# Performance work log

Hardware: AMD Instinct MI355X
Metric: run time of the kernel (lower is better)

The kernel has to match this reference:

```python
import jax, jax.numpy as jnp
import numpy as np

IN_CH = 1024
INTER_CH = 512
NUM_EXPERTS = 128
B, S = 16, 4096  # T = B*S = 65536 tokens, 512 tokens/expert


def setup_inputs() -> dict:
    key = jax.random.key(0)
    kx, kp, k1w, k1b, k2w, k2b, k3w, k3b = jax.random.split(key, 8)
    T = B * S
    x = jax.random.normal(kx, (B, S, IN_CH), dtype=jnp.float32)
    # Mirror torch: indices = randperm(T) % E; idxs = indices.argsort() (stable)
    perm = jax.random.permutation(kp, T)
    expert_assign = perm % NUM_EXPERTS
    idxs = jnp.argsort(expert_assign, stable=True).astype(jnp.int64)
    # BatchLinear params initialized with randn, matching the torch module
    w1_w = jax.random.normal(k1w, (NUM_EXPERTS, INTER_CH, IN_CH), dtype=jnp.float32)
    w1_b = jax.random.normal(k1b, (NUM_EXPERTS, INTER_CH), dtype=jnp.float32)
    w2_w = jax.random.normal(k2w, (NUM_EXPERTS, IN_CH, INTER_CH), dtype=jnp.float32)
    w2_b = jax.random.normal(k2b, (NUM_EXPERTS, IN_CH), dtype=jnp.float32)
    w3_w = jax.random.normal(k3w, (NUM_EXPERTS, INTER_CH, IN_CH), dtype=jnp.float32)
    w3_b = jax.random.normal(k3b, (NUM_EXPERTS, INTER_CH), dtype=jnp.float32)
    return {"x": x, "idxs": idxs, "w1_w": w1_w, "w1_b": w1_b,
            "w2_w": w2_w, "w2_b": w2_b, "w3_w": w3_w, "w3_b": w3_b}


def reference(x, idxs, w1_w, w1_b, w2_w, w2_b, w3_w, w3_b):
    Bx, Sx, C = x.shape
    E = w1_w.shape[0]
    xf = x.reshape(Bx * Sx, C)            # [T, C]
    # dispatch: gather tokens grouped by expert -> [E, T/E, C]
    xs = xf[idxs].reshape(E, -1, C)
    # SwiGLU FFN, batched over experts
    h1 = jnp.einsum('etc,efc->etf', xs, w1_w) + w1_b[:, None, :]  # [E, T/E, F]
    h3 = jnp.einsum('etc,efc->etf', xs, w3_w) + w3_b[:, None, :]
    h = jax.nn.silu(h1) * h3
    out = jnp.einsum('etf,ecf->etc', h, w2_w) + w2_b[:, None, :]  # [E, T/E, C]
    # combine: scatter tokens back to original order
    out = out.reshape(Bx * Sx, C)
    inv = jnp.argsort(idxs)
    return out[inv].reshape(Bx, Sx, C)
```

## Files before the change

### kernel.cpp

```cpp
#include <hip/hip_runtime.h>

#define IN_CH 1024
#define INTER 512
#define NEXP  128
#define TPE   512

typedef __bf16 bf16x8  __attribute__((ext_vector_type(8)));
typedef __bf16 bf16x4v __attribute__((ext_vector_type(4)));
typedef float  f32x4   __attribute__((ext_vector_type(4)));

#define GLOAD(dst, p) \
  asm volatile("global_load_dwordx4 %0, %1, off" : "=&v"(dst) : "v"(p))

#define VM_WAIT() do { \
  asm volatile("s_waitcnt vmcnt(0)" ::: "memory"); \
  __builtin_amdgcn_sched_barrier(0); } while (0)

#define PHASE_SYNC() do { \
  __builtin_amdgcn_s_barrier(); \
  asm volatile("s_waitcnt lgkmcnt(0)" ::: "memory"); \
  __builtin_amdgcn_sched_barrier(0); \
  __builtin_amdgcn_s_setprio(1); } while (0)
#define PHASE_END() do { \
  __builtin_amdgcn_s_setprio(0); \
  __builtin_amdgcn_s_barrier(); } while (0)

#define GLDS16(gsrc, ldst) \
  __builtin_amdgcn_global_load_lds( \
      (const __attribute__((address_space(1))) unsigned int*)(gsrc), \
      (__attribute__((address_space(3))) unsigned int*)(ldst), 16, 0, 0)

__global__ __launch_bounds__(512) void moe_h_kernel(
    const float* __restrict__ x, const int* __restrict__ idxs,
    const float* __restrict__ w1w, const float* __restrict__ w1b,
    const float* __restrict__ w3w, const float* __restrict__ w3b,
    __bf16* __restrict__ hbuf)
{
  __shared__ __align__(16) ushort sA [2][128*64];
  __shared__ __align__(16) ushort sB1[2][128*64];
  __shared__ __align__(16) ushort sB3[2][128*64];

  const int blk = (blockIdx.x & 7) * (NEXP*16/8) + (blockIdx.x >> 3);
  const int e   = blk >> 4;
  const int tl  = blk & 15;
  const int tm  = tl >> 2, tn = tl & 3;

  const int tid  = threadIdx.x;
  const int lane = tid & 63;
  const int wid  = tid >> 6;
  const int wm   = wid >> 1;
  const int wn   = wid & 1;

  const int rA = tid >> 3;
  const int c  = tid & 7;
  const int swzc = ((c ^ (rA&7))<<3);
  const int so0 = rA*64 + swzc;
  const int so1 = (rA+64)*64 + swzc;

  const int tok0 = idxs[e*TPE + tm*128 + rA];
  const int tok1 = idxs[e*TPE + tm*128 + rA + 64];
  const float* ap0 = x + (size_t)tok0*IN_CH + (c<<3);
  const float* ap1 = x + (size_t)tok1*IN_CH + (c<<3);
  const float* q0p = w1w + ((size_t)e*INTER + tn*128 + rA)*IN_CH + (c<<3);
  const float* q1p = q0p + (size_t)64*IN_CH;
  const float* t0p = w3w + ((size_t)e*INTER + tn*128 + rA)*IN_CH + (c<<3);
  const float* t1p = t0p + (size_t)64*IN_CH;

  f32x4 acc1[2][4], acc3[2][4];
#pragma unroll
  for (int a = 0; a < 2; ++a)
#pragma unroll
    for (int b = 0; b < 4; ++b) {
      acc1[a][b] = (f32x4){0.f,0.f,0.f,0.f};
      acc3[a][b] = (f32x4){0.f,0.f,0.f,0.f};
    }

  f32x4 a0l,a0h, a1l,a1h, q0l,q0h, q1l,q1h, t0l,t0h, t1l,t1h;

  auto loads = [&](int kof) {
    GLOAD(a0l, ap0 + kof); GLOAD(a0h, ap0 + kof + 4);
    GLOAD(a1l, ap1 + kof); GLOAD(a1h, ap1 + kof + 4);
    GLOAD(q0l, q0p + kof); GLOAD(q0h, q0p + kof + 4);
    GLOAD(q1l, q1p + kof); GLOAD(q1h, q1p + kof + 4);
    GLOAD(t0l, t0p + kof); GLOAD(t0h, t0p + kof + 4);
    GLOAD(t1l, t1p + kof); GLOAD(t1h, t1p + kof + 4);
  };
  auto cvt8 = [](const f32x4& lo, const f32x4& hi) {
    bf16x8 r;
    r[0]=(__bf16)lo[0]; r[1]=(__bf16)lo[1]; r[2]=(__bf16)lo[2]; r[3]=(__bf16)lo[3];
    r[4]=(__bf16)hi[0]; r[5]=(__bf16)hi[1]; r[6]=(__bf16)hi[2]; r[7]=(__bf16)hi[3];
    return r;
  };
  auto stores = [&](int buf) {
    VM_WAIT();
    *(bf16x8*)&sA [buf][so0] = cvt8(a0l, a0h);
    *(bf16x8*)&sA [buf][so1] = cvt8(a1l, a1h);
    *(bf16x8*)&sB1[buf][so0] = cvt8(q0l, q0h);
    *(bf16x8*)&sB1[buf][so1] = cvt8(q1l, q1h);
    *(bf16x8*)&sB3[buf][so0] = cvt8(t0l, t0h);
    *(bf16x8*)&sB3[buf][so1] = cvt8(t1l, t1h);
  };
  auto mfma_tile = [&](int buf) {
#pragma unroll
    for (int ks = 0; ks < 2; ++ks) {
      bf16x8 af[2], bq[4], bt[4];
      const int k8 = (ks<<2) + (lane>>4);
#pragma unroll
      for (int mi = 0; mi < 2; ++mi) {
        const int r = wm*32 + mi*16 + (lane&15);
        af[mi] = *(const bf16x8*)&sA[buf][r*64 + ((k8 ^ (r&7))<<3)];
      }
#pragma unroll
      for (int ni = 0; ni < 4; ++ni) {
        const int r   = wn*64 + ni*16 + (lane&15);
        const int off = r*64 + ((k8 ^ (r&7))<<3);
        bq[ni] = *(const bf16x8*)&sB1[buf][off];
        bt[ni] = *(const bf16x8*)&sB3[buf][off];
      }
#pragma unroll
      for (int mi = 0; mi < 2; ++mi)
#pragma unroll
        for (int ni = 0; ni < 4; ++ni) {
          acc1[mi][ni] = __builtin_amdgcn_mfma_f32_16x16x32_bf16(af[mi], bq[ni], acc1[mi][ni], 0, 0, 0);
          acc3[mi][ni] = __builtin_amdgcn_mfma_f32_16x16x32_bf16(af[mi], bt[ni], acc3[mi][ni], 0, 0, 0);
        }
    }
  };

  loads(0);
  stores(0);
  loads(64);
  asm volatile("s_waitcnt lgkmcnt(0)" ::: "memory");
  __builtin_amdgcn_s_barrier();

  int cur = 0;
  const int NT = IN_CH/64;
  for (int kt = 0; kt < NT; ++kt) {
    if (kt < NT - 1) stores(cur ^ 1);
    if (kt < NT - 2) loads((kt+2)*64);
    __builtin_amdgcn_s_setprio(1);
    mfma_tile(cur);
    __builtin_amdgcn_s_setprio(0);
    asm volatile("s_waitcnt lgkmcnt(0)" ::: "memory");
    __builtin_amdgcn_s_barrier();
    cur ^= 1;
  }

  const int rowbase = tm*128 + wm*32;
  const int colbase = tn*128 + wn*64;
#pragma unroll
  for (int ni = 0; ni < 4; ++ni) {
    const int fc = colbase + ni*16 + (lane&15);
    const float b1v = w1b[e*INTER + fc];
    const float b3v = w3b[e*INTER + fc];
#pragma unroll
    for (int mi = 0; mi < 2; ++mi) {
#pragma unroll
      for (int j = 0; j < 4; ++j) {
        const int rl = rowbase + mi*16 + ((lane>>4)<<2) + j;
        const float h1 = acc1[mi][ni][j] + b1v;
        const float h3 = acc3[mi][ni][j] + b3v;
        const float s  = h1 / (1.0f + __expf(-h1));
        hbuf[((size_t)e*TPE + rl)*INTER + fc] = (__bf16)(s * h3);
      }
    }
  }
}

__global__ __launch_bounds__(512) void moe_out_kernel(
    const __bf16* __restrict__ hbuf, const float* __restrict__ w2w,
    const float* __restrict__ w2b, const int* __restrict__ idxs,
    float* __restrict__ out)
{
  __shared__ __align__(16) ushort sA[2][128*64];
  __shared__ __align__(16) ushort sB[2][128*64];

  const int blk = (blockIdx.x & 7) * (NEXP*32/8) + (blockIdx.x >> 3);
  const int e   = blk >> 5;
  const int tl  = blk & 31;
  const int tm  = tl >> 3, tn = tl & 7;

  const int tid  = threadIdx.x;
  const int lane = tid & 63;
  const int wid  = tid >> 6;
  const int wm   = wid >> 1;
  const int wn   = wid & 1;

  const int arow0 = wid*16 + (lane>>3);
  const int asc0  = (lane&7) ^ (arow0&7);
  const int asc1  = (lane&7) ^ ((arow0+8)&7);
  const __bf16* ag0 = hbuf + ((size_t)e*TPE + tm*128 + arow0    )*INTER + (asc0<<3);
  const __bf16* ag1 = hbuf + ((size_t)e*TPE + tm*128 + arow0 + 8)*INTER + (asc1<<3);
  const int aslot0 = (wid*128)      * 8;
  const int aslot1 = (wid*128 + 64) * 8;

  const int r0   = tid >> 4;
  const int c4   = tid & 15;
  const int swzB = ((((c4>>1) ^ (r0&7))<<3) | ((c4&1)<<2));
  const float* bp = w2w + ((size_t)e*IN_CH + tn*128 + r0)*INTER + (c4<<2);

  f32x4 acc[2][4];
#pragma unroll
  for (int a = 0; a < 2; ++a)
#pragma unroll
    for (int b = 0; b < 4; ++b) acc[a][b] = (f32x4){0.f,0.f,0.f,0.f};

  float4 wv[4];

  auto gldsA = [&](int buf, int kof) {
    GLDS16(ag0 + kof, &sA[buf][aslot0]);
    GLDS16(ag1 + kof, &sA[buf][aslot1]);
  };
  auto loadsB = [&](int kof) {
#pragma unroll
    for (int i = 0; i < 4; ++i)
      wv[i] = *(const float4*)(bp + (size_t)(32*i)*INTER + kof);
  };
  auto storesB = [&](int buf) {
#pragma unroll
    for (int i = 0; i < 4; ++i) {
      bf16x4v b;
      b[0]=(__bf16)wv[i].x; b[1]=(__bf16)wv[i].y; b[2]=(__bf16)wv[i].z; b[3]=(__bf16)wv[i].w;
      *(bf16x4v*)&sB[buf][(r0 + 32*i)*64 + swzB] = b;
    }
  };
  auto rdA = [&](int buf, int ks, bf16x8 af[2]) {
    const int k8 = (ks<<2) + (lane>>4);
#pragma unroll
    for (int mi = 0; mi < 2; ++mi) {
      const int r = wm*32 + mi*16 + (lane&15);
      af[mi] = *(const bf16x8*)&sA[buf][r*64 + ((k8 ^ (r&7))<<3)];
    }
  };
  auto rdB = [&](int buf, int ks, bf16x8 bfr[4]) {
    const int k8 = (ks<<2) + (lane>>4);
#pragma unroll
    for (int ni = 0; ni < 4; ++ni) {
      const int r = wn*64 + ni*16 + (lane&15);
      bfr[ni] = *(const bf16x8*)&sB[buf][r*64 + ((k8 ^ (r&7))<<3)];
    }
  };

  gldsA(0, 0);
  loadsB(0);
  VM_WAIT();
  storesB(0);
  loadsB(64);
  asm volatile("s_waitcnt lgkmcnt(0)" ::: "memory");
  __builtin_amdgcn_s_barrier();

  int cur = 0;
  const int NT = INTER/64;
  for (int kt = 0; kt < NT; ++kt) {
    bf16x8 af[2], bfr[4];

    rdA(cur, 0, af);
    rdB(cur, 0, bfr);
    if (kt < NT - 1) {
      VM_WAIT();
      storesB(cur ^ 1);
      gldsA(cur ^ 1, (kt+1)*64);
      __builtin_amdgcn_sched_barrier(0);
    }
    if (kt < NT - 2) loadsB((kt+2)*64);
    PHASE_SYNC();
#pragma unroll
    for (int mi = 0; mi < 2; ++mi)
#pragma unroll
      for (int ni = 0; ni < 4; ++ni)
        acc[mi][ni] = __builtin_amdgcn_mfma_f32_16x16x32_bf16(af[mi], bfr[ni], acc[mi][ni], 0, 0, 0);
    PHASE_END();

    rdA(cur, 1, af);
    rdB(cur, 1, bfr);
    PHASE_SYNC();
#pragma unroll
    for (int mi = 0; mi < 2; ++mi)
#pragma unroll
      for (int ni = 0; ni < 4; ++ni)
        acc[mi][ni] = __builtin_amdgcn_mfma_f32_16x16x32_bf16(af[mi], bfr[ni], acc[mi][ni], 0, 0, 0);
    __builtin_amdgcn_s_setprio(0);
    if (kt < NT - 2)      asm volatile("s_waitcnt vmcnt(4)" ::: "memory");
    else if (kt < NT - 1) asm volatile("s_waitcnt vmcnt(0)" ::: "memory");
    __builtin_amdgcn_s_barrier();

    cur ^= 1;
  }

  const int rowbase = tm*128 + wm*32;
  const int colbase = tn*128 + wn*64;
  float b2v[4];
#pragma unroll
  for (int ni = 0; ni < 4; ++ni)
    b2v[ni] = w2b[e*IN_CH + colbase + ni*16 + (lane&15)];
#pragma unroll
  for (int mi = 0; mi < 2; ++mi) {
#pragma unroll
    for (int j = 0; j < 4; ++j) {
      const int rl  = rowbase + mi*16 + ((lane>>4)<<2) + j;
      const int tok = idxs[e*TPE + rl];
      float* orow = out + (size_t)tok*IN_CH;
#pragma unroll
      for (int ni = 0; ni < 4; ++ni)
        orow[colbase + ni*16 + (lane&15)] = acc[mi][ni][j] + b2v[ni];
    }
  }
}

extern "C" void kernel_launch(void* const* d_in, const int* in_sizes, int n_in,
                              void* d_out, int out_size, void* d_ws, size_t ws_size,
                              hipStream_t stream) {
  const float* x    = (const float*)d_in[0];
  const int*   idxs = (const int*)d_in[1];
  const float* w1w  = (const float*)d_in[2];
  const float* w1b  = (const float*)d_in[3];
  const float* w2w  = (const float*)d_in[4];
  const float* w2b  = (const float*)d_in[5];
  const float* w3w  = (const float*)d_in[6];
  const float* w3b  = (const float*)d_in[7];
  float*  out  = (float*)d_out;
  __bf16* hbuf = (__bf16*)d_ws;

  moe_h_kernel<<<dim3(NEXP*16), dim3(512), 0, stream>>>(x, idxs, w1w, w1b, w3w, w3b, hbuf);
  moe_out_kernel<<<dim3(NEXP*32), dim3(512), 0, stream>>>(hbuf, w2w, w2b, idxs, out);
}
```

Before: 483.5 us.

## Pre-convert x to bf16 and use direct-to-LDS gathers with narrower N tiles

Adds a separate pass that converts the whole fp32 activation tensor to bf16 in workspace. The first GEMM kernel can then gather token rows straight into LDS with global_load_lds instead of loading and converting them in registers. The tile shape changes from 128x128 to 128x64 per block, so twice as many blocks run and LDS use is smaller. The cost is an extra full read and write of x (about 384MB of traffic). The new path runs only when the workspace is large enough, and otherwise falls back to the old kernel.

```diff
diff --git a/kernel.cpp b/kernel.cpp
--- a/kernel.cpp
+++ b/kernel.cpp
@@ -4,6 +4,7 @@
 #define INTER 512
 #define NEXP  128
 #define TPE   512
+#define TTOT  (NEXP*TPE)
 
 typedef __bf16 bf16x8  __attribute__((ext_vector_type(8)));
 typedef __bf16 bf16x4v __attribute__((ext_vector_type(4)));
@@ -29,6 +30,181 @@
   __builtin_amdgcn_global_load_lds( \
       (const __attribute__((address_space(1))) unsigned int*)(gsrc), \
       (__attribute__((address_space(3))) unsigned int*)(ldst), 16, 0, 0)
+
+__global__ __launch_bounds__(256) void xcvt_kernel(
+    const float* __restrict__ x, __bf16* __restrict__ xbf)
+{
+  const long n8 = (long)TTOT * IN_CH / 8;
+  long i = (long)blockIdx.x * 256 + threadIdx.x;
+  const long stride = (long)gridDim.x * 256;
+  for (; i < n8; i += stride) {
+    const float4 lo = *(const float4*)(x + i*8);
+    const float4 hi = *(const float4*)(x + i*8 + 4);
+    bf16x8 r;
+    r[0]=(__bf16)lo.x; r[1]=(__bf16)lo.y; r[2]=(__bf16)lo.z; r[3]=(__bf16)lo.w;
+    r[4]=(__bf16)hi.x; r[5]=(__bf16)hi.y; r[6]=(__bf16)hi.z; r[7]=(__bf16)hi.w;
+    *(bf16x8*)(xbf + i*8) = r;
+  }
+}
+
+__global__ __launch_bounds__(512) void moe_h2_kernel(
+    const __bf16* __restrict__ xbf, const int* __restrict__ idxs,
+    const float* __restrict__ w1w, const float* __restrict__ w1b,
+    const float* __restrict__ w3w, const float* __restrict__ w3b,
+    __bf16* __restrict__ hbuf)
+{
+  __shared__ __align__(16) ushort sA [2][128*64];
+  __shared__ __align__(16) ushort sB1[2][64*64];
+  __shared__ __align__(16) ushort sB3[2][64*64];
+
+  const int blk = (blockIdx.x & 7) * (NEXP*32/8) + (blockIdx.x >> 3);
+  const int e   = blk >> 5;
+  const int tl  = blk & 31;
+  const int tm  = tl >> 3, tn = tl & 7;
+
+  const int tid  = threadIdx.x;
+  const int lane = tid & 63;
+  const int wid  = tid >> 6;
+  const int wm   = wid >> 1;
+  const int wn   = wid & 1;
+
+  const int arow0 = wid*16 + (lane>>3);
+  const int asc0  = (lane&7) ^ (arow0&7);
+  const int asc1  = (lane&7) ^ ((arow0+8)&7);
+  const int tokA0 = idxs[e*TPE + tm*128 + arow0];
+  const int tokA1 = idxs[e*TPE + tm*128 + arow0 + 8];
+  const __bf16* ag0 = xbf + (size_t)tokA0*IN_CH + (asc0<<3);
+  const __bf16* ag1 = xbf + (size_t)tokA1*IN_CH + (asc1<<3);
+  const int aslot0 = (wid*128)      * 8;
+  const int aslot1 = (wid*128 + 64) * 8;
+
+  const int r0   = tid >> 4;
+  const int c4   = tid & 15;
+  const int swzB = ((((c4>>1) ^ (r0&7))<<3) | ((c4&1)<<2));
+  const float* b1p = w1w + ((size_t)e*INTER + tn*64 + r0)*IN_CH + (c4<<2);
+  const float* b3p = w3w + ((size_t)e*INTER + tn*64 + r0)*IN_CH + (c4<<2);
+
+  f32x4 acc1[2][2], acc3[2][2];
+#pragma unroll
+  for (int a = 0; a < 2; ++a)
+#pragma unroll
+    for (int b = 0; b < 2; ++b) {
+      acc1[a][b] = (f32x4){0.f,0.f,0.f,0.f};
+      acc3[a][b] = (f32x4){0.f,0.f,0.f,0.f};
+    }
+
+  float4 wv1[2], wv3[2];
+
+  auto gldsA = [&](int buf, int kof) {
+    GLDS16(ag0 + kof, &sA[buf][aslot0]);
+    GLDS16(ag1 + kof, &sA[buf][aslot1]);
+  };
+  auto loadsB = [&](int kof) {
+    wv1[0] = *(const float4*)(b1p + kof);
+    wv1[1] = *(const float4*)(b1p + (size_t)32*IN_CH + kof);
+    wv3[0] = *(const float4*)(b3p + kof);
+    wv3[1] = *(const float4*)(b3p + (size_t)32*IN_CH + kof);
+  };
+  auto cvt4 = [](const float4& v) {
+    bf16x4v b;
+    b[0]=(__bf16)v.x; b[1]=(__bf16)v.y; b[2]=(__bf16)v.z; b[3]=(__bf16)v.w;
+    return b;
+  };
+  auto storesB = [&](int buf) {
+    *(bf16x4v*)&sB1[buf][ r0      *64 + swzB] = cvt4(wv1[0]);
+    *(bf16x4v*)&sB1[buf][(r0 + 32)*64 + swzB] = cvt4(wv1[1]);
+    *(bf16x4v*)&sB3[buf][ r0      *64 + swzB] = cvt4(wv3[0]);
+    *(bf16x4v*)&sB3[buf][(r0 + 32)*64 + swzB] = cvt4(wv3[1]);
+  };
+  auto rdA = [&](int buf, int ks, bf16x8 af[2]) {
+    const int k8 = (ks<<2) + (lane>>4);
+#pragma unroll
+    for (int mi = 0; mi < 2; ++mi) {
+      const int r = wm*32 + mi*16 + (lane&15);
+      af[mi] = *(const bf16x8*)&sA[buf][r*64 + ((k8 ^ (r&7))<<3)];
+    }
+  };
+  auto rdB = [&](int buf, int ks, bf16x8 bq[2], bf16x8 bt[2]) {
+    const int k8 = (ks<<2) + (lane>>4);
+#pragma unroll
+    for (int ni = 0; ni < 2; ++ni) {
+      const int r   = wn*32 + ni*16 + (lane&15);
+      const int off = r*64 + ((k8 ^ (r&7))<<3);
+      bq[ni] = *(const bf16x8*)&sB1[buf][off];
+      bt[ni] = *(const bf16x8*)&sB3[buf][off];
+    }
+  };
+
+  gldsA(0, 0);
+  loadsB(0);
+  VM_WAIT();
+  storesB(0);
+  loadsB(64);
+  asm volatile("s_waitcnt lgkmcnt(0)" ::: "memory");
+  __builtin_amdgcn_s_barrier();
+
+  int cur = 0;
+  const int NT = IN_CH/64;
+  for (int kt = 0; kt < NT; ++kt) {
+    bf16x8 af[2], bq[2], bt[2];
+
+    rdA(cur, 0, af);
+    rdB(cur, 0, bq, bt);
+    if (kt < NT - 1) {
+      VM_WAIT();
+      storesB(cur ^ 1);
+      gldsA(cur ^ 1, (kt+1)*64);
+      __builtin_amdgcn_sched_barrier(0);
+    }
+    if (kt < NT - 2) loadsB((kt+2)*64);
+    PHASE_SYNC();
+#pragma unroll
+    for (int mi = 0; mi < 2; ++mi)
+#pragma unroll
+      for (int ni = 0; ni < 2; ++ni) {
+        acc1[mi][ni] = __builtin_amdgcn_mfma_f32_16x16x32_bf16(af[mi], bq[ni], acc1[mi][ni], 0, 0, 0);
+        acc3[mi][ni] = __builtin_amdgcn_mfma_f32_16x16x32_bf16(af[mi], bt[ni], acc3[mi][ni], 0, 0, 0);
+      }
+    PHASE_END();
+
+    rdA(cur, 1, af);
+    rdB(cur, 1, bq, bt);
+    PHASE_SYNC();
+#pragma unroll
+    for (int mi = 0; mi < 2; ++mi)
+#pragma unroll
+      for (int ni = 0; ni < 2; ++ni) {
+        acc1[mi][ni] = __builtin_amdgcn_mfma_f32_16x16x32_bf16(af[mi], bq[ni], acc1[mi][ni], 0, 0, 0);
+        acc3[mi][ni] = __builtin_amdgcn_mfma_f32_16x16x32_bf16(af[mi], bt[ni], acc3[mi][ni], 0, 0, 0);
+      }
+    __builtin_amdgcn_s_setprio(0);
+    if (kt < NT - 2)      asm volatile("s_waitcnt vmcnt(4)" ::: "memory");
+    else if (kt < NT - 1) asm volatile("s_waitcnt vmcnt(0)" ::: "memory");
+    __builtin_amdgcn_s_barrier();
+
+    cur ^= 1;
+  }
+
+  const int rowbase = tm*128 + wm*32;
+  const int colbase = tn*64  + wn*32;
+#pragma unroll
+  for (int ni = 0; ni < 2; ++ni) {
+    const int fc = colbase + ni*16 + (lane&15);
+    const float b1v = w1b[e*INTER + fc];
+    const float b3v = w3b[e*INTER + fc];
+#pragma unroll
+    for (int mi = 0; mi < 2; ++mi) {
+#pragma unroll
+      for (int j = 0; j < 4; ++j) {
+        const int rl = rowbase + mi*16 + ((lane>>4)<<2) + j;
+        const float h1 = acc1[mi][ni][j] + b1v;
+        const float h3 = acc3[mi][ni][j] + b3v;
+        const float s  = h1 / (1.0f + __expf(-h1));
+        hbuf[((size_t)e*TPE + rl)*INTER + fc] = (__bf16)(s * h3);
+      }
+    }
+  }
+}
 
 __global__ __launch_bounds__(512) void moe_h_kernel(
     const float* __restrict__ x, const int* __restrict__ idxs,
@@ -318,9 +494,24 @@
   const float* w2b  = (const float*)d_in[5];
   const float* w3w  = (const float*)d_in[6];
   const float* w3b  = (const float*)d_in[7];
-  float*  out  = (float*)d_out;
-  __bf16* hbuf = (__bf16*)d_ws;
-
-  moe_h_kernel<<<dim3(NEXP*16), dim3(512), 0, stream>>>(x, idxs, w1w, w1b, w3w, w3b, hbuf);
-  moe_out_kernel<<<dim3(NEXP*32), dim3(512), 0, stream>>>(hbuf, w2w, w2b, idxs, out);
+  float* out = (float*)d_out;
+
+  const size_t XBF = (size_t)TTOT * IN_CH * sizeof(__bf16);
+  const size_t HB  = (size_t)NEXP * TPE * INTER * sizeof(__bf16);
+
+  if (ws_size >= XBF + HB) {
+    __bf16* xbf  = (__bf16*)d_ws;
+    __bf16* hbuf = (__bf16*)((char*)d_ws + XBF);
+    xcvt_kernel<<<dim3(2048), dim3(256), 0, stream>>>(x, xbf);
+    moe_h2_kernel<<<dim3(NEXP*32), dim3(512), 0, stream>>>(
+        xbf, idxs, w1w, w1b, w3w, w3b, hbuf);
+    moe_out_kernel<<<dim3(NEXP*32), dim3(512), 0, stream>>>(
+        hbuf, w2w, w2b, idxs, out);
+  } else {
+    __bf16* hbuf = (__bf16*)d_ws;
+    moe_h_kernel<<<dim3(NEXP*16), dim3(512), 0, stream>>>(
+        x, idxs, w1w, w1b, w3w, w3b, hbuf);
+    moe_out_kernel<<<dim3(NEXP*32), dim3(512), 0, stream>>>(
+        hbuf, w2w, w2b, idxs, out);
+  }
 }
```

After: 510.2 us. +5.5%, slower.
